# Kernel optimization log

Measured on AMD Instinct MI355X. Metric: run time of the kernel, lower is better.

The kernel has to match this reference:

```python
import jax, jax.numpy as jnp
import numpy as np

B, D, C = 4096, 1024, 11003
SCALE = 28.0
EPS_LS = 0.1
T = 4.0
L2, L3, L4 = 1.0, 1.0, 1.0
ALPHA, BETA = 0.6, 0.4
SPOS, SNEG = 10.0, 40.0
HDR_ALPHA, HDR_BETA, PLEN = 3.0, 3.0, 63


def setup_inputs() -> dict:
    key = jax.random.key(0)
    k1, k2, k3, k4, k5 = jax.random.split(key, 5)
    return {
        "visual_embed": jax.random.normal(k1, (B, D), dtype=jnp.float32),
        "textual_embed": jax.random.normal(k2, (B, D), dtype=jnp.float32),
        "labels": jax.random.randint(k3, (B,), 0, C, dtype=jnp.int64)
        if jax.config.read("jax_enable_x64") else jax.random.randint(k3, (B,), 0, C, dtype=jnp.int32),
        "W": jax.random.normal(k4, (D, C), dtype=jnp.float32) * (6.0 / (D + C)) ** 0.5,
        "W_text": jax.random.normal(k5, (D, C), dtype=jnp.float32) * (6.0 / (D + C)) ** 0.5,
    }


def _l2norm(x, axis):
    return x / jnp.linalg.norm(x, axis=axis, keepdims=True)


def _label_smooth_ce(logits, labels):
    # CrossEntropyLabelSmooth with epsilon=0.1
    lp = jax.nn.log_softmax(logits, axis=1)
    n, c = logits.shape
    picked = jnp.take_along_axis(lp, labels[:, None], axis=1)[:, 0]
    return -((1.0 - EPS_LS) * picked + (EPS_LS / c) * lp.sum(axis=1)).mean()


def _pdist(e, eps=1e-12):
    sq = (e * e).sum(axis=1)
    d2 = jnp.maximum(sq[:, None] + sq[None, :] - 2.0 * (e @ e.T), eps)
    d = jnp.sqrt(d2)
    return d * (1.0 - jnp.eye(e.shape[0], dtype=d.dtype))  # zero diagonal


def _hard_dark_rank(student, teacher):
    score_t = -HDR_ALPHA * _pdist(teacher) ** HDR_BETA
    score_s = -HDR_ALPHA * _pdist(student) ** HDR_BETA
    # top PLEN neighbors of teacher (skip self at rank 0), descending sort
    permute_idx = jnp.argsort(-score_t, axis=1)[:, 1 : PLEN + 1]  # [B, PLEN]
    ordered = jnp.take_along_axis(score_s, permute_idx, axis=1)  # [B, PLEN]
    # logsumexp over suffixes ordered[:, i:] == reversed cumulative logsumexp
    rev = jnp.flip(ordered, axis=1)
    lse_tail = jnp.flip(jax.lax.cumlogsumexp(rev, axis=1), axis=1)
    log_prob = (ordered - lse_tail).sum(axis=1)
    return (-log_prob).mean()


def _kl_div(student_logits, teacher_logits):
    s = jax.nn.softmax(student_logits / T, axis=1)
    t = jax.nn.softmax(jax.lax.stop_gradient(teacher_logits) / T, axis=1)
    log_s = jnp.log(jnp.maximum(s, 1e-12))
    log_t = jnp.log(jnp.maximum(t, 1e-12))
    return (((log_t - log_s) * t).sum(axis=1)).mean()


def reference(visual_embed, textual_embed, labels, W, W_text):
    vn = _l2norm(visual_embed, axis=1)
    tn = _l2norm(textual_embed, axis=1)
    Wn = W / jnp.linalg.norm(W, axis=0, keepdims=True)
    Wtn = W_text / jnp.linalg.norm(W_text, axis=0, keepdims=True)

    visual_logits = SCALE * (vn @ Wn)   # [B, C]
    textual_logits = SCALE * (tn @ Wn)  # [B, C]

    v_loss = _label_smooth_ce(visual_logits, labels)
    t_loss = _label_smooth_ce(textual_logits, labels)

    # distillation (LAMBDA2 feature L2 + LAMBDA3 KL on logits)
    vf = jax.lax.stop_gradient(vn)
    dist_f = ((vf - tn) ** 2).sum(axis=1).mean()
    dist_p = _kl_div(textual_logits, visual_logits)
    distillation = L2 * dist_f + L3 * dist_p

    # W_text filter CE (LAMBDA4 branch)
    t_filter = L4 * _label_smooth_ce(SCALE * (tn @ Wtn), labels)

    # HardDarkRank (Flickr30K branch): student=textual, teacher=detached visual
    loss_hdr = _hard_dark_rank(tn, jax.lax.stop_gradient(vn))

    instance = v_loss + t_loss + t_filter + distillation + 0.1 * loss_hdr

    # global_align_loss, fully vectorized. The original loops over rows AND
    # columns so every (i,j) pair is counted twice.
    sim = vn @ tn.T  # [B, B]
    mask = labels[:, None] == labels[None, :]
    loss_pos = jnp.log1p(jnp.exp(-SPOS * (sim - ALPHA)))
    loss_neg = jnp.log1p(jnp.exp(SNEG * (sim - BETA)))
    global_align = 2.0 * jnp.where(mask, loss_pos, loss_neg).sum() / sim.shape[0]

    return instance + global_align
```

## Files before the change

kernel.cpp:

```cpp
#include <hip/hip_runtime.h>
#include <math.h>

#define Bn 4096
#define Dn 1024
#define Cn 11003
#define Cpad 11008
#define NCTL 86
#define NQ 9
#define NT 32
#define NTRI 528

typedef __attribute__((ext_vector_type(8))) short bf16x8;
typedef __attribute__((ext_vector_type(4))) float f32x4;
typedef __attribute__((ext_vector_type(16))) float f32x16;

__device__ __forceinline__ unsigned short f2bf(float f) {
  union { float f; unsigned u; } v; v.f = f;
  unsigned r = (v.u + 0x7fffu + ((v.u >> 16) & 1u)) >> 16;
  return (unsigned short)r;
}
__device__ __forceinline__ float bf2f(unsigned short h) {
  union { unsigned u; float f; } v; v.u = ((unsigned)h) << 16;
  return v.f;
}

__device__ __forceinline__ void stage16(const unsigned short* g, unsigned short* l) {
  __builtin_amdgcn_global_load_lds(
      (const __attribute__((address_space(1))) void*)g,
      (__attribute__((address_space(3))) void*)l, 16, 0, 0);
}

#define SRC_BLK(tid) (((tid) & 7) ^ (((tid) >> 3) & 7))
#define FRAG(buf, R, KB) (*(const bf16x8*)((buf) + (R) * 64 + (((KB) ^ ((R) & 7)) * 8)))

__device__ __forceinline__ float blk_sum256(float v, volatile float* sb) {
#pragma unroll
  for (int o = 32; o > 0; o >>= 1) v += __shfl_down(v, o, 64);
  __syncthreads();
  if ((threadIdx.x & 63) == 0) sb[threadIdx.x >> 6] = v;
  __syncthreads();
  return sb[0] + sb[1] + sb[2] + sb[3];
}

__global__ void zero_acc_k(float* acc) {
  if (threadIdx.x < 8) acc[threadIdx.x] = 0.f;
}

__global__ __launch_bounds__(256) void rownorm_k(const float* __restrict__ xv,
                                                 const float* __restrict__ xt,
                                                 unsigned short* __restrict__ yv,
                                                 unsigned short* __restrict__ yt,
                                                 float* __restrict__ sqv,
                                                 float* __restrict__ sqt) {
  __shared__ float sb[4];
  const float* x = blockIdx.y ? xt : xv;
  unsigned short* y = blockIdx.y ? yt : yv;
  float* sq = blockIdx.y ? sqt : sqv;
  int r = blockIdx.x;
  const float* xr = x + (size_t)r * Dn;
  float s = 0.f;
  for (int k = threadIdx.x; k < Dn; k += 256) { float v = xr[k]; s += v * v; }
  s = blk_sum256(s, sb);
  float nrm = sqrtf(s);
  float s2 = 0.f;
  for (int k = threadIdx.x; k < Dn; k += 256) {
    float v = xr[k] / nrm;
    y[(size_t)r * Dn + k] = f2bf(v);
    s2 += v * v;
  }
  s2 = blk_sum256(s2, sb);
  if (threadIdx.x == 0) sq[r] = s2;
}

__global__ __launch_bounds__(256) void colnorm_k(const float* __restrict__ W,
                                                 const float* __restrict__ Wt,
                                                 float* __restrict__ rnW,
                                                 float* __restrict__ rnWt) {
  const float* X = blockIdx.y ? Wt : W;
  float* rn = blockIdx.y ? rnWt : rnW;
  int c = blockIdx.x * 256 + threadIdx.x;
  if (c >= Cn) return;
  float s = 0.f;
  for (int d = 0; d < Dn; ++d) { float v = X[(size_t)d * Cn + c]; s += v * v; }
  rn[c] = 1.f / sqrtf(s);
}

__global__ __launch_bounds__(256) void transpose_k(const float* __restrict__ W,
                                                   const float* __restrict__ Wt,
                                                   const float* __restrict__ rnW,
                                                   const float* __restrict__ rnWt,
                                                   unsigned short* __restrict__ WnT,
                                                   unsigned short* __restrict__ WtnT) {
  __shared__ float T[64][65];
  const float* X = blockIdx.z ? Wt : W;
  const float* rn = blockIdx.z ? rnWt : rnW;
  unsigned short* WT = blockIdx.z ? WtnT : WnT;
  const int c0 = blockIdx.x * 64, d0 = blockIdx.y * 64;
  const int tid = threadIdx.x;
  const int cl = tid & 63;
  for (int dl = tid >> 6; dl < 64; dl += 4) {
    float v = (c0 + cl < Cn) ? X[(size_t)(d0 + dl) * Cn + c0 + cl] : 0.f;
    T[cl][dl] = v;
  }
  __syncthreads();
  const int dd = tid & 63;
  for (int co = tid >> 6; co < 64; co += 4) {
    int c = c0 + co;
    unsigned short o = 0;
    if (c < Cn) o = f2bf(T[co][dd] * rn[c]);
    WT[(size_t)c * Dn + d0 + dd] = o;
  }
}

__global__ __launch_bounds__(256, 2) void logits_vt_k(
    const unsigned short* __restrict__ vnh, const unsigned short* __restrict__ tnh,
    const unsigned short* __restrict__ WnT, float* __restrict__ part) {
  __shared__ __align__(16) unsigned short Av[128 * 64];
  __shared__ __align__(16) unsigned short At[128 * 64];
  __shared__ __align__(16) unsigned short Bs[128 * 64];
  __shared__ float qsum[7 * 128];

  const int rt = blockIdx.x, ct = blockIdx.y;
  const int r0 = rt * 128, c0 = ct * 128;
  const int tid = threadIdx.x;
  const int lane = tid & 63;
  const int wid = tid >> 6;
  const int wr = (wid >> 1) * 64, wc = (wid & 1) * 64;
  const int l31 = lane & 31, half = lane >> 5;

  for (int t = tid; t < 7 * 128; t += 256) qsum[t] = 0.f;

  f32x16 accV[2][2], accT[2][2];
#pragma unroll
  for (int i = 0; i < 2; ++i)
#pragma unroll
    for (int j = 0; j < 2; ++j)
#pragma unroll
      for (int e = 0; e < 16; ++e) { accV[i][j][e] = 0.f; accT[i][j][e] = 0.f; }

  const int srow = tid >> 3;
  const int skc = SRC_BLK(tid) * 8;

  for (int kk = 0; kk < 16; ++kk) {
    const int k0 = kk * 64;
#pragma unroll
    for (int p = 0; p < 4; ++p) {
      stage16(vnh + (size_t)(r0 + p * 32 + srow) * Dn + k0 + skc, Av + p * 2048 + tid * 8);
      stage16(tnh + (size_t)(r0 + p * 32 + srow) * Dn + k0 + skc, At + p * 2048 + tid * 8);
      stage16(WnT + (size_t)(c0 + p * 32 + srow) * Dn + k0 + skc, Bs + p * 2048 + tid * 8);
    }
    __syncthreads();
#pragma unroll
    for (int t = 0; t < 4; ++t) {
      const int KB = t * 2 + half;
      bf16x8 av[2], at[2], bb[2];
#pragma unroll
      for (int f = 0; f < 2; ++f) {
        av[f] = FRAG(Av, wr + f * 32 + l31, KB);
        at[f] = FRAG(At, wr + f * 32 + l31, KB);
        bb[f] = FRAG(Bs, wc + f * 32 + l31, KB);
      }
#pragma unroll
      for (int i = 0; i < 2; ++i)
#pragma unroll
        for (int j = 0; j < 2; ++j) {
          accV[i][j] = __builtin_amdgcn_mfma_f32_32x32x16_bf16(av[i], bb[j], accV[i][j], 0, 0, 0);
          accT[i][j] = __builtin_amdgcn_mfma_f32_32x32x16_bf16(at[i], bb[j], accT[i][j], 0, 0, 0);
        }
    }
    __syncthreads();
  }

#pragma unroll
  for (int bi = 0; bi < 2; ++bi) {
#pragma unroll
    for (int r = 0; r < 16; ++r) {
      const int rowl = wr + bi * 32 + (r & 3) + 8 * (r >> 2) + 4 * half;
      float s0 = 0.f, s1 = 0.f, s2 = 0.f, s3 = 0.f, s6 = 0.f, s7 = 0.f, s8 = 0.f;
#pragma unroll
      for (int bj = 0; bj < 2; ++bj) {
        int col = c0 + wc + bj * 32 + l31;
        if (col < Cn) {
          float V = 28.f * accV[bi][bj][r];
          float T = 28.f * accT[bi][bj][r];
          float ev4 = __expf((V - 28.f) * 0.25f);
          float et4 = __expf((T - 28.f) * 0.25f);
          float ev2 = ev4 * ev4, et2 = et4 * et4;
          s0 += ev2 * ev2;
          s1 += V;
          s2 += et2 * et2;
          s3 += T;
          s6 += ev4;
          s7 += et4;
          s8 += ev4 * (V - T);
        }
      }
#pragma unroll
      for (int o = 1; o < 32; o <<= 1) {
        s0 += __shfl_xor(s0, o, 64); s1 += __shfl_xor(s1, o, 64);
        s2 += __shfl_xor(s2, o, 64); s3 += __shfl_xor(s3, o, 64);
        s6 += __shfl_xor(s6, o, 64); s7 += __shfl_xor(s7, o, 64);
        s8 += __shfl_xor(s8, o, 64);
      }
      if (l31 == 0) {
        atomicAdd(&qsum[0 * 128 + rowl], s0);
        atomicAdd(&qsum[1 * 128 + rowl], s1);
        atomicAdd(&qsum[2 * 128 + rowl], s2);
        atomicAdd(&qsum[3 * 128 + rowl], s3);
        atomicAdd(&qsum[4 * 128 + rowl], s6);
        atomicAdd(&qsum[5 * 128 + rowl], s7);
        atomicAdd(&qsum[6 * 128 + rowl], s8);
      }
    }
  }
  __syncthreads();
  if (tid < 128) {
    size_t base = (size_t)ct * Bn + r0 + tid;
    const size_t qs = (size_t)NCTL * Bn;
    part[0 * qs + base] = qsum[0 * 128 + tid];
    part[1 * qs + base] = qsum[1 * 128 + tid];
    part[2 * qs + base] = qsum[2 * 128 + tid];
    part[3 * qs + base] = qsum[3 * 128 + tid];
    part[6 * qs + base] = qsum[4 * 128 + tid];
    part[7 * qs + base] = qsum[5 * 128 + tid];
    part[8 * qs + base] = qsum[6 * 128 + tid];
  }
}

__global__ __launch_bounds__(256, 2) void logits_f_k(
    const unsigned short* __restrict__ tnh, const unsigned short* __restrict__ WtnT,
    float* __restrict__ part) {
  __shared__ __align__(16) unsigned short Aa[256 * 64];
  __shared__ __align__(16) unsigned short Bs[128 * 64];
  __shared__ float qsum[2 * 256];

  const int rt = blockIdx.x, ct = blockIdx.y;
  const int r0 = rt * 256, c0 = ct * 128;
  const int tid = threadIdx.x;
  const int lane = tid & 63;
  const int wid = tid >> 6;
  const int wr = (wid >> 1) * 128, wc = (wid & 1) * 64;
  const int l31 = lane & 31, half = lane >> 5;

  for (int t = tid; t < 2 * 256; t += 256) qsum[t] = 0.f;

  f32x16 acc[4][2];
#pragma unroll
  for (int i = 0; i < 4; ++i)
#pragma unroll
    for (int j = 0; j < 2; ++j)
#pragma unroll
      for (int e = 0; e < 16; ++e) acc[i][j][e] = 0.f;

  const int srow = tid >> 3;
  const int skc = SRC_BLK(tid) * 8;

  for (int kk = 0; kk < 16; ++kk) {
    const int k0 = kk * 64;
#pragma unroll
    for (int p = 0; p < 8; ++p)
      stage16(tnh + (size_t)(r0 + p * 32 + srow) * Dn + k0 + skc, Aa + p * 2048 + tid * 8);
#pragma unroll
    for (int p = 0; p < 4; ++p)
      stage16(WtnT + (size_t)(c0 + p * 32 + srow) * Dn + k0 + skc, Bs + p * 2048 + tid * 8);
    __syncthreads();
#pragma unroll
    for (int t = 0; t < 4; ++t) {
      const int KB = t * 2 + half;
      bf16x8 aa[4], bb[2];
#pragma unroll
      for (int f = 0; f < 4; ++f) aa[f] = FRAG(Aa, wr + f * 32 + l31, KB);
#pragma unroll
      for (int f = 0; f < 2; ++f) bb[f] = FRAG(Bs, wc + f * 32 + l31, KB);
#pragma unroll
      for (int i = 0; i < 4; ++i)
#pragma unroll
        for (int j = 0; j < 2; ++j)
          acc[i][j] = __builtin_amdgcn_mfma_f32_32x32x16_bf16(aa[i], bb[j], acc[i][j], 0, 0, 0);
    }
    __syncthreads();
  }

#pragma unroll
  for (int bi = 0; bi < 4; ++bi) {
#pragma unroll
    for (int r = 0; r < 16; ++r) {
      const int rowl = wr + bi * 32 + (r & 3) + 8 * (r >> 2) + 4 * half;
      float s4 = 0.f, s5 = 0.f;
#pragma unroll
      for (int bj = 0; bj < 2; ++bj) {
        int col = c0 + wc + bj * 32 + l31;
        if (col < Cn) {
          float F = 28.f * acc[bi][bj][r];
          s4 += __expf(F - 28.f);
          s5 += F;
        }
      }
#pragma unroll
      for (int o = 1; o < 32; o <<= 1) {
        s4 += __shfl_xor(s4, o, 64);
        s5 += __shfl_xor(s5, o, 64);
      }
      if (l31 == 0) {
        atomicAdd(&qsum[0 * 256 + rowl], s4);
        atomicAdd(&qsum[1 * 256 + rowl], s5);
      }
    }
  }
  __syncthreads();
  {
    size_t base = (size_t)ct * Bn + r0 + tid;
    const size_t qs = (size_t)NCTL * Bn;
    part[4 * qs + base] = qsum[0 * 256 + tid];
    part[5 * qs + base] = qsum[1 * 256 + tid];
  }
}

__global__ __launch_bounds__(256, 2) void gramv_align_k(
    const unsigned short* __restrict__ vnh, const unsigned short* __restrict__ tnh,
    const int* __restrict__ labels, float* __restrict__ G, float* __restrict__ accbuf) {
  __shared__ __align__(16) unsigned short Aa[128 * 64];
  __shared__ __align__(16) unsigned short Vb[128 * 64];
  __shared__ __align__(16) unsigned short Tb[128 * 64];
  __shared__ int li_s[128], lj_s[128];
  __shared__ float sb[4];
  const int jt = blockIdx.x, it = blockIdx.y;
  const int j0 = jt * 128, i0 = it * 128;
  const int tid = threadIdx.x;
  const int lane = tid & 63;
  const int wid = tid >> 6;
  const int wr = (wid >> 1) * 64, wc = (wid & 1) * 64;
  const int m = lane & 15, q = lane >> 4;

  if (tid < 128) li_s[tid] = labels[i0 + tid];
  else lj_s[tid - 128] = labels[j0 + tid - 128];

  const f32x4 zero4 = {0.f, 0.f, 0.f, 0.f};
  f32x4 accG[4][4], accS[4][4];
#pragma unroll
  for (int i = 0; i < 4; ++i)
#pragma unroll
    for (int j = 0; j < 4; ++j) { accG[i][j] = zero4; accS[i][j] = zero4; }

  const int srow = tid >> 3;
  const int skc = SRC_BLK(tid) * 8;

  for (int kk = 0; kk < 16; ++kk) {
    const int k0 = kk * 64;
#pragma unroll
    for (int p = 0; p < 4; ++p) {
      stage16(vnh + (size_t)(i0 + p * 32 + srow) * Dn + k0 + skc, Aa + p * 2048 + tid * 8);
      stage16(vnh + (size_t)(j0 + p * 32 + srow) * Dn + k0 + skc, Vb + p * 2048 + tid * 8);
      stage16(tnh + (size_t)(j0 + p * 32 + srow) * Dn + k0 + skc, Tb + p * 2048 + tid * 8);
    }
    __syncthreads();
#pragma unroll
    for (int ks = 0; ks < 2; ++ks) {
      const int KB = ks * 4 + q;
      bf16x8 aa[4], vb[4], tb[4];
#pragma unroll
      for (int f = 0; f < 4; ++f) {
        aa[f] = FRAG(Aa, wr + f * 16 + m, KB);
        vb[f] = FRAG(Vb, wc + f * 16 + m, KB);
        tb[f] = FRAG(Tb, wc + f * 16 + m, KB);
      }
#pragma unroll
      for (int i = 0; i < 4; ++i)
#pragma unroll
        for (int j = 0; j < 4; ++j) {
          accG[i][j] = __builtin_amdgcn_mfma_f32_16x16x32_bf16(aa[i], vb[j], accG[i][j], 0, 0, 0);
          accS[i][j] = __builtin_amdgcn_mfma_f32_16x16x32_bf16(aa[i], tb[j], accS[i][j], 0, 0, 0);
        }
    }
    __syncthreads();
  }

  float ls = 0.f;
#pragma unroll
  for (int i = 0; i < 4; ++i)
#pragma unroll
    for (int r = 0; r < 4; ++r) {
      int rowl = wr + i * 16 + q * 4 + r;
      int li = li_s[rowl];
#pragma unroll
      for (int j = 0; j < 4; ++j) {
        int coll = wc + j * 16 + m;
        G[(size_t)(i0 + rowl) * Bn + j0 + coll] = accG[i][j][r];
        int lj = lj_s[coll];
        float s = accS[i][j][r];
        float x = (li == lj) ? (-10.f * (s - 0.6f)) : (40.f * (s - 0.4f));
        ls += fmaxf(x, 0.f) + __logf(1.f + __expf(-fabsf(x)));
      }
    }
  float tot = blk_sum256(ls, sb);
  if (tid == 0) atomicAdd(&accbuf[1], tot);
}

__global__ __launch_bounds__(256, 3) void gramsym_bf16_k(const unsigned short* __restrict__ A,
                                                         unsigned short* __restrict__ G) {
  __shared__ __align__(16) unsigned short Aa[128 * 64];
  __shared__ __align__(16) unsigned short Bs[128 * 64];
  int t = blockIdx.x, it = 0, rem = NT;
  while (t >= rem) { t -= rem; ++it; --rem; }
  const int jt = it + t;
  const int i0 = it * 128, j0 = jt * 128;
  const int tid = threadIdx.x;
  const int lane = tid & 63;
  const int wid = tid >> 6;
  const int wr = (wid >> 1) * 64, wc = (wid & 1) * 64;
  const int m = lane & 15, q = lane >> 4;

  const f32x4 zero4 = {0.f, 0.f, 0.f, 0.f};
  f32x4 acc[4][4];
#pragma unroll
  for (int i = 0; i < 4; ++i)
#pragma unroll
    for (int j = 0; j < 4; ++j) acc[i][j] = zero4;

  const int srow = tid >> 3;
  const int skc = SRC_BLK(tid) * 8;

  for (int kk = 0; kk < 16; ++kk) {
    const int k0 = kk * 64;
#pragma unroll
    for (int p = 0; p < 4; ++p) {
      stage16(A + (size_t)(i0 + p * 32 + srow) * Dn + k0 + skc, Aa + p * 2048 + tid * 8);
      stage16(A + (size_t)(j0 + p * 32 + srow) * Dn + k0 + skc, Bs + p * 2048 + tid * 8);
    }
    __syncthreads();
#pragma unroll
    for (int ks = 0; ks < 2; ++ks) {
      const int KB = ks * 4 + q;
      bf16x8 aa[4], bb[4];
#pragma unroll
      for (int f = 0; f < 4; ++f) {
        aa[f] = FRAG(Aa, wr + f * 16 + m, KB);
        bb[f] = FRAG(Bs, wc + f * 16 + m, KB);
      }
#pragma unroll
      for (int i = 0; i < 4; ++i)
#pragma unroll
        for (int j = 0; j < 4; ++j)
          acc[i][j] = __builtin_amdgcn_mfma_f32_16x16x32_bf16(aa[i], bb[j], acc[i][j], 0, 0, 0);
    }
    __syncthreads();
  }
#pragma unroll
  for (int i = 0; i < 4; ++i)
#pragma unroll
    for (int j = 0; j < 4; ++j)
#pragma unroll
      for (int r = 0; r < 4; ++r) {
        int row = wr + i * 16 + q * 4 + r, col = wc + j * 16 + m;
        unsigned short h = f2bf(acc[i][j][r]);
        G[(size_t)(i0 + row) * Bn + j0 + col] = h;
        if (it != jt) G[(size_t)(j0 + col) * Bn + i0 + row] = h;
      }
}

__global__ __launch_bounds__(256) void picked_k(const unsigned short* __restrict__ vnh,
                                                const unsigned short* __restrict__ tnh,
                                                const unsigned short* __restrict__ WnT,
                                                const unsigned short* __restrict__ WtnT,
                                                const int* __restrict__ labels,
                                                float* __restrict__ pv, float* __restrict__ pt,
                                                float* __restrict__ pf, float* __restrict__ df) {
  __shared__ float sb[4];
  int r = blockIdx.x;
  int lab = labels[r];
  float spv = 0.f, spt = 0.f, spf = 0.f, sdf = 0.f;
  for (int k = threadIdx.x; k < Dn; k += 256) {
    float a = bf2f(vnh[(size_t)r * Dn + k]);
    float b = bf2f(tnh[(size_t)r * Dn + k]);
    float w = bf2f(WnT[(size_t)lab * Dn + k]);
    float wt = bf2f(WtnT[(size_t)lab * Dn + k]);
    spv += a * w;
    spt += b * w;
    spf += b * wt;
    float dd = a - b;
    sdf += dd * dd;
  }
  spv = blk_sum256(spv, sb);
  spt = blk_sum256(spt, sb);
  spf = blk_sum256(spf, sb);
  sdf = blk_sum256(sdf, sb);
  if (threadIdx.x == 0) {
    pv[r] = 28.f * spv;
    pt[r] = 28.f * spt;
    pf[r] = 28.f * spf;
    df[r] = sdf;
  }
}

__global__ __launch_bounds__(256) void finalize_k(const float* __restrict__ part,
                                                  const float* __restrict__ pv,
                                                  const float* __restrict__ pt,
                                                  const float* __restrict__ pf,
                                                  const float* __restrict__ df,
                                                  float* __restrict__ accbuf) {
  __shared__ float sb[4];
  int r = blockIdx.x * 256 + threadIdx.x;
  float s[NQ];
#pragma unroll
  for (int q = 0; q < NQ; ++q) s[q] = 0.f;
  const size_t qs = (size_t)NCTL * Bn;
  for (int ct = 0; ct < NCTL; ++ct) {
#pragma unroll
    for (int q = 0; q < NQ; ++q) s[q] += part[(size_t)q * qs + (size_t)ct * Bn + r];
  }
  float lseV = logf(s[0]) + 28.f;
  float lseT = logf(s[2]) + 28.f;
  float lseF = logf(s[4]) + 28.f;
  const float invC = 1.f / (float)Cn;
  float ceV = -(0.9f * (pv[r] - lseV) + 0.1f * invC * (s[1] - (float)Cn * lseV));
  float ceT = -(0.9f * (pt[r] - lseT) + 0.1f * invC * (s[3] - (float)Cn * lseT));
  float ceF = -(0.9f * (pf[r] - lseF) + 0.1f * invC * (s[5] - (float)Cn * lseF));
  float kl = s[8] / (4.f * s[6]) + logf(s[7]) - logf(s[6]);
  float row = ceV + ceT + ceF + kl + df[r];
  float tot = blk_sum256(row, sb);
  if (threadIdx.x == 0) atomicAdd(&accbuf[0], tot / (float)Bn);
}

__device__ __forceinline__ int kswz(int j) {
  return (j & ~63) | ((j ^ (j >> 6)) & 63);
}
__device__ __forceinline__ unsigned long long shflx_u64(unsigned long long v, int o) {
  int lo = __shfl_xor((int)(unsigned)v, o, 64);
  int hi = __shfl_xor((int)(unsigned)(v >> 32), o, 64);
  return ((unsigned long long)(unsigned)hi << 32) | (unsigned)lo;
}

__global__ __launch_bounds__(256) void hdr_k(const float* __restrict__ Gv,
                                             const unsigned short* __restrict__ Gtb,
                                             const float* __restrict__ sqv,
                                             const float* __restrict__ sqt,
                                             float* __restrict__ accbuf) {
  __shared__ float key[Bn];
  __shared__ int selIdx[64];
  __shared__ float selS[64];
  const int i = blockIdx.x, tid = threadIdx.x;
  const int lane = tid & 63, wid = tid >> 6;
  const float INF = __builtin_inff();
  float sqi = sqv[i];
  const float4* gv4 = (const float4*)(Gv + (size_t)i * Bn);
  const float4* sq4 = (const float4*)sqv;
  for (int j4 = tid; j4 < Bn / 4; j4 += 256) {
    float4 g = gv4[j4];
    float4 s = sq4[j4];
    int j = j4 * 4;
    key[kswz(j + 0)] = (j + 0 == i) ? INF : fmaxf(sqi + s.x - 2.f * g.x, 1e-12f);
    key[kswz(j + 1)] = (j + 1 == i) ? INF : fmaxf(sqi + s.y - 2.f * g.y, 1e-12f);
    key[kswz(j + 2)] = (j + 2 == i) ? INF : fmaxf(sqi + s.z - 2.f * g.z, 1e-12f);
    key[kswz(j + 3)] = (j + 3 == i) ? INF : fmaxf(sqi + s.w - 2.f * g.w, 1e-12f);
  }
  __syncthreads();

  if (wid == 0) {
    unsigned long long best = ~0ull;
    for (int k = 0; k < 64; ++k) {
      int j = k * 64 + lane;
      float v = key[kswz(j)];
      unsigned long long p = ((unsigned long long)__float_as_uint(v) << 32) | (unsigned)j;
      if (p < best) best = p;
    }
    for (int it = 0; it < 63; ++it) {
      unsigned long long w = best;
#pragma unroll
      for (int o = 32; o > 0; o >>= 1) {
        unsigned long long ow = shflx_u64(w, o);
        if (ow < w) w = ow;
      }
      int bj = (int)(unsigned)w;
      if (lane == 0) selIdx[it] = bj;
      int s = bj & 63;
      int kj = (lane << 6) | s;
      int sidx = kswz(kj);
      float kv = key[sidx];
      if (kj == bj) { kv = INF; key[sidx] = INF; }
      unsigned long long p = ((unsigned long long)__float_as_uint(kv) << 32) | (unsigned)kj;
#pragma unroll
      for (int o = 32; o > 0; o >>= 1) {
        unsigned long long op = shflx_u64(p, o);
        if (op < p) p = op;
      }
      if (lane == s) best = p;
    }
  }
  __syncthreads();

  if (tid < 63) {
    int j = selIdx[tid];
    float g = bf2f(Gtb[(size_t)i * Bn + j]);
    float d2 = fmaxf(sqt[i] + sqt[j] - 2.f * g, 1e-12f);
    selS[tid] = -3.f * sqrtf(d2) * d2;
  }
  __syncthreads();

  if (tid == 0) {
    float lse = selS[62];
    float loss = 0.f;
    for (int k = 61; k >= 0; --k) {
      float a = fmaxf(lse, selS[k]);
      lse = a + logf(__expf(lse - a) + __expf(selS[k] - a));
      loss += lse - selS[k];
    }
    atomicAdd(&accbuf[2], loss);
  }
}

__global__ void combine_k(const float* __restrict__ accbuf, float* __restrict__ out) {
  out[0] = accbuf[0] + (2.f / (float)Bn) * accbuf[1] + (0.1f / (float)Bn) * accbuf[2];
}

extern "C" void kernel_launch(void* const* d_in, const int* in_sizes, int n_in,
                              void* d_out, int out_size, void* d_ws, size_t ws_size,
                              hipStream_t stream) {
  const float* ve = (const float*)d_in[0];
  const float* te = (const float*)d_in[1];
  const int* labels = (const int*)d_in[2];
  const float* W = (const float*)d_in[3];
  const float* Wt = (const float*)d_in[4];
  float* out = (float*)d_out;

  char* base = (char*)d_ws;
  size_t off = 0;
  unsigned short* vnh = (unsigned short*)(base + off);  off += (size_t)Bn * Dn * 2;
  unsigned short* tnh = (unsigned short*)(base + off);  off += (size_t)Bn * Dn * 2;
  unsigned short* WnT = (unsigned short*)(base + off);  off += (size_t)Cpad * Dn * 2;
  unsigned short* WtnT = (unsigned short*)(base + off); off += (size_t)Cpad * Dn * 2;
  float* Gv = (float*)(base + off);          off += (size_t)Bn * Bn * 4;
  unsigned short* Gtb = (unsigned short*)(base + off); off += (size_t)Bn * Bn * 2;
  float* part = (float*)(base + off);        off += (size_t)NQ * NCTL * Bn * 4;
  float* rnW = (float*)(base + off);         off += (size_t)Cpad * 4;
  float* rnWt = (float*)(base + off);        off += (size_t)Cpad * 4;
  float* sqv = (float*)(base + off);         off += (size_t)Bn * 4;
  float* sqt = (float*)(base + off);         off += (size_t)Bn * 4;
  float* pv = (float*)(base + off);          off += (size_t)Bn * 4;
  float* pt = (float*)(base + off);          off += (size_t)Bn * 4;
  float* pf = (float*)(base + off);          off += (size_t)Bn * 4;
  float* df = (float*)(base + off);          off += (size_t)Bn * 4;
  float* acc = (float*)(base + off);         off += 64;

  zero_acc_k<<<1, 64, 0, stream>>>(acc);
  rownorm_k<<<dim3(Bn, 2), 256, 0, stream>>>(ve, te, vnh, tnh, sqv, sqt);
  colnorm_k<<<dim3((Cn + 255) / 256, 2), 256, 0, stream>>>(W, Wt, rnW, rnWt);
  transpose_k<<<dim3(Cpad / 64, Dn / 64, 2), 256, 0, stream>>>(W, Wt, rnW, rnWt, WnT, WtnT);
  logits_vt_k<<<dim3(Bn / 128, NCTL), 256, 0, stream>>>(vnh, tnh, WnT, part);
  logits_f_k<<<dim3(Bn / 256, NCTL), 256, 0, stream>>>(tnh, WtnT, part);
  gramv_align_k<<<dim3(NT, NT), 256, 0, stream>>>(vnh, tnh, labels, Gv, acc);
  gramsym_bf16_k<<<NTRI, 256, 0, stream>>>(tnh, Gtb);
  picked_k<<<Bn, 256, 0, stream>>>(vnh, tnh, WnT, WtnT, labels, pv, pt, pf, df);
  finalize_k<<<Bn / 256, 256, 0, stream>>>(part, pv, pt, pf, df, acc);
  hdr_k<<<Bn, 256, 0, stream>>>(Gv, Gtb, sqv, sqt, acc);
  combine_k<<<1, 1, 0, stream>>>(acc, out);
}
```

Before: 1.026 ms.

## Compute logit row sums via column-sum of W and switch to 16x16 MFMA

Row sums of the logits (needed for label smoothing) are now computed algebraically as the dot product of each normalized embedding with the column-sum of the bf16 normalized weight, accumulated during the transpose. This drops three per-element sum reductions and their partial buffers from the GEMM epilogues. Separately, the logits GEMMs switch from 32x32x16 to 16x16x32 MFMA tiles, which changes register layout and the epilogue shuffle width. The column-sum uses atomics and reassociates the sum, so rounding differs slightly.

```diff
diff --git a/kernel.cpp b/kernel.cpp
--- a/kernel.cpp
+++ b/kernel.cpp
@@ -6,13 +6,12 @@
 #define Cn 11003
 #define Cpad 11008
 #define NCTL 86
-#define NQ 9
+#define NQ 6
 #define NT 32
 #define NTRI 528
 
 typedef __attribute__((ext_vector_type(8))) short bf16x8;
 typedef __attribute__((ext_vector_type(4))) float f32x4;
-typedef __attribute__((ext_vector_type(16))) float f32x16;
 
 __device__ __forceinline__ unsigned short f2bf(float f) {
   union { float f; unsigned u; } v; v.f = f;
@@ -42,8 +41,10 @@
   return sb[0] + sb[1] + sb[2] + sb[3];
 }
 
-__global__ void zero_acc_k(float* acc) {
-  if (threadIdx.x < 8) acc[threadIdx.x] = 0.f;
+__global__ void zero_acc_k(float* acc, float* cw, float* cwt) {
+  int tid = threadIdx.x;
+  for (int i = tid; i < Dn; i += 256) { cw[i] = 0.f; cwt[i] = 0.f; }
+  if (tid < 8) acc[tid] = 0.f;
 }
 
 __global__ __launch_bounds__(256) void rownorm_k(const float* __restrict__ xv,
@@ -90,26 +91,36 @@
                                                    const float* __restrict__ rnW,
                                                    const float* __restrict__ rnWt,
                                                    unsigned short* __restrict__ WnT,
-                                                   unsigned short* __restrict__ WtnT) {
+                                                   unsigned short* __restrict__ WtnT,
+                                                   float* __restrict__ cw,
+                                                   float* __restrict__ cwt) {
   __shared__ float T[64][65];
+  __shared__ float cwp[64];
   const float* X = blockIdx.z ? Wt : W;
   const float* rn = blockIdx.z ? rnWt : rnW;
   unsigned short* WT = blockIdx.z ? WtnT : WnT;
+  float* cwg = blockIdx.z ? cwt : cw;
   const int c0 = blockIdx.x * 64, d0 = blockIdx.y * 64;
   const int tid = threadIdx.x;
   const int cl = tid & 63;
+  if (tid < 64) cwp[tid] = 0.f;
   for (int dl = tid >> 6; dl < 64; dl += 4) {
     float v = (c0 + cl < Cn) ? X[(size_t)(d0 + dl) * Cn + c0 + cl] : 0.f;
     T[cl][dl] = v;
   }
   __syncthreads();
   const int dd = tid & 63;
+  float ls = 0.f;
   for (int co = tid >> 6; co < 64; co += 4) {
     int c = c0 + co;
     unsigned short o = 0;
     if (c < Cn) o = f2bf(T[co][dd] * rn[c]);
     WT[(size_t)c * Dn + d0 + dd] = o;
-  }
+    ls += bf2f(o);
+  }
+  atomicAdd(&cwp[dd], ls);
+  __syncthreads();
+  if (tid < 64) atomicAdd(&cwg[d0 + tid], cwp[tid]);
 }
 
 __global__ __launch_bounds__(256, 2) void logits_vt_k(
@@ -118,7 +129,7 @@
   __shared__ __align__(16) unsigned short Av[128 * 64];
   __shared__ __align__(16) unsigned short At[128 * 64];
   __shared__ __align__(16) unsigned short Bs[128 * 64];
-  __shared__ float qsum[7 * 128];
+  __shared__ float qsum[5 * 128];
 
   const int rt = blockIdx.x, ct = blockIdx.y;
   const int r0 = rt * 128, c0 = ct * 128;
@@ -126,17 +137,16 @@
   const int lane = tid & 63;
   const int wid = tid >> 6;
   const int wr = (wid >> 1) * 64, wc = (wid & 1) * 64;
-  const int l31 = lane & 31, half = lane >> 5;
-
-  for (int t = tid; t < 7 * 128; t += 256) qsum[t] = 0.f;
-
-  f32x16 accV[2][2], accT[2][2];
-#pragma unroll
-  for (int i = 0; i < 2; ++i)
-#pragma unroll
-    for (int j = 0; j < 2; ++j)
-#pragma unroll
-      for (int e = 0; e < 16; ++e) { accV[i][j][e] = 0.f; accT[i][j][e] = 0.f; }
+  const int m = lane & 15, q = lane >> 4;
+
+  for (int t = tid; t < 5 * 128; t += 256) qsum[t] = 0.f;
+
+  const f32x4 zero4 = {0.f, 0.f, 0.f, 0.f};
+  f32x4 accV[4][4], accT[4][4];
+#pragma unroll
+  for (int i = 0; i < 4; ++i)
+#pragma unroll
+    for (int j = 0; j < 4; ++j) { accV[i][j] = zero4; accT[i][j] = zero4; }
 
   const int srow = tid >> 3;
   const int skc = SRC_BLK(tid) * 8;
@@ -151,65 +161,60 @@
     }
     __syncthreads();
 #pragma unroll
-    for (int t = 0; t < 4; ++t) {
-      const int KB = t * 2 + half;
-      bf16x8 av[2], at[2], bb[2];
-#pragma unroll
-      for (int f = 0; f < 2; ++f) {
-        av[f] = FRAG(Av, wr + f * 32 + l31, KB);
-        at[f] = FRAG(At, wr + f * 32 + l31, KB);
-        bb[f] = FRAG(Bs, wc + f * 32 + l31, KB);
-      }
-#pragma unroll
-      for (int i = 0; i < 2; ++i)
-#pragma unroll
-        for (int j = 0; j < 2; ++j) {
-          accV[i][j] = __builtin_amdgcn_mfma_f32_32x32x16_bf16(av[i], bb[j], accV[i][j], 0, 0, 0);
-          accT[i][j] = __builtin_amdgcn_mfma_f32_32x32x16_bf16(at[i], bb[j], accT[i][j], 0, 0, 0);
+    for (int ks = 0; ks < 2; ++ks) {
+      const int KB = ks * 4 + q;
+      bf16x8 av[4], at[4], bb[4];
+#pragma unroll
+      for (int f = 0; f < 4; ++f) {
+        av[f] = FRAG(Av, wr + f * 16 + m, KB);
+        at[f] = FRAG(At, wr + f * 16 + m, KB);
+        bb[f] = FRAG(Bs, wc + f * 16 + m, KB);
+      }
+#pragma unroll
+      for (int i = 0; i < 4; ++i)
+#pragma unroll
+        for (int j = 0; j < 4; ++j) {
+          accV[i][j] = __builtin_amdgcn_mfma_f32_16x16x32_bf16(av[i], bb[j], accV[i][j], 0, 0, 0);
+          accT[i][j] = __builtin_amdgcn_mfma_f32_16x16x32_bf16(at[i], bb[j], accT[i][j], 0, 0, 0);
         }
     }
     __syncthreads();
   }
 
 #pragma unroll
-  for (int bi = 0; bi < 2; ++bi) {
-#pragma unroll
-    for (int r = 0; r < 16; ++r) {
-      const int rowl = wr + bi * 32 + (r & 3) + 8 * (r >> 2) + 4 * half;
-      float s0 = 0.f, s1 = 0.f, s2 = 0.f, s3 = 0.f, s6 = 0.f, s7 = 0.f, s8 = 0.f;
-#pragma unroll
-      for (int bj = 0; bj < 2; ++bj) {
-        int col = c0 + wc + bj * 32 + l31;
+  for (int i = 0; i < 4; ++i) {
+#pragma unroll
+    for (int r = 0; r < 4; ++r) {
+      const int rowl = wr + i * 16 + q * 4 + r;
+      float s0 = 0.f, s2 = 0.f, s6 = 0.f, s7 = 0.f, s8 = 0.f;
+#pragma unroll
+      for (int j = 0; j < 4; ++j) {
+        int col = c0 + wc + j * 16 + m;
         if (col < Cn) {
-          float V = 28.f * accV[bi][bj][r];
-          float T = 28.f * accT[bi][bj][r];
+          float V = 28.f * accV[i][j][r];
+          float T = 28.f * accT[i][j][r];
           float ev4 = __expf((V - 28.f) * 0.25f);
           float et4 = __expf((T - 28.f) * 0.25f);
           float ev2 = ev4 * ev4, et2 = et4 * et4;
           s0 += ev2 * ev2;
-          s1 += V;
           s2 += et2 * et2;
-          s3 += T;
           s6 += ev4;
           s7 += et4;
           s8 += ev4 * (V - T);
         }
       }
 #pragma unroll
-      for (int o = 1; o < 32; o <<= 1) {
-        s0 += __shfl_xor(s0, o, 64); s1 += __shfl_xor(s1, o, 64);
-        s2 += __shfl_xor(s2, o, 64); s3 += __shfl_xor(s3, o, 64);
+      for (int o = 1; o < 16; o <<= 1) {
+        s0 += __shfl_xor(s0, o, 64); s2 += __shfl_xor(s2, o, 64);
         s6 += __shfl_xor(s6, o, 64); s7 += __shfl_xor(s7, o, 64);
         s8 += __shfl_xor(s8, o, 64);
       }
-      if (l31 == 0) {
+      if (m == 0) {
         atomicAdd(&qsum[0 * 128 + rowl], s0);
-        atomicAdd(&qsum[1 * 128 + rowl], s1);
-        atomicAdd(&qsum[2 * 128 + rowl], s2);
-        atomicAdd(&qsum[3 * 128 + rowl], s3);
-        atomicAdd(&qsum[4 * 128 + rowl], s6);
-        atomicAdd(&qsum[5 * 128 + rowl], s7);
-        atomicAdd(&qsum[6 * 128 + rowl], s8);
+        atomicAdd(&qsum[1 * 128 + rowl], s2);
+        atomicAdd(&qsum[2 * 128 + rowl], s6);
+        atomicAdd(&qsum[3 * 128 + rowl], s7);
+        atomicAdd(&qsum[4 * 128 + rowl], s8);
       }
     }
   }
@@ -219,11 +224,9 @@
     const size_t qs = (size_t)NCTL * Bn;
     part[0 * qs + base] = qsum[0 * 128 + tid];
     part[1 * qs + base] = qsum[1 * 128 + tid];
-    part[2 * qs + base] = qsum[2 * 128 + tid];
-    part[3 * qs + base] = qsum[3 * 128 + tid];
-    part[6 * qs + base] = qsum[4 * 128 + tid];
-    part[7 * qs + base] = qsum[5 * 128 + tid];
-    part[8 * qs + base] = qsum[6 * 128 + tid];
+    part[3 * qs + base] = qsum[2 * 128 + tid];
+    part[4 * qs + base] = qsum[3 * 128 + tid];
+    part[5 * qs + base] = qsum[4 * 128 + tid];
   }
 }
 
@@ -232,7 +235,7 @@
     float* __restrict__ part) {
   __shared__ __align__(16) unsigned short Aa[256 * 64];
   __shared__ __align__(16) unsigned short Bs[128 * 64];
-  __shared__ float qsum[2 * 256];
+  __shared__ float qsum[256];
 
   const int rt = blockIdx.x, ct = blockIdx.y;
   const int r0 = rt * 256, c0 = ct * 128;
@@ -240,17 +243,16 @@
   const int lane = tid & 63;
   const int wid = tid >> 6;
   const int wr = (wid >> 1) * 128, wc = (wid & 1) * 64;
-  const int l31 = lane & 31, half = lane >> 5;
-
-  for (int t = tid; t < 2 * 256; t += 256) qsum[t] = 0.f;
-
-  f32x16 acc[4][2];
-#pragma unroll
-  for (int i = 0; i < 4; ++i)
-#pragma unroll
-    for (int j = 0; j < 2; ++j)
-#pragma unroll
-      for (int e = 0; e < 16; ++e) acc[i][j][e] = 0.f;
+  const int m = lane & 15, q = lane >> 4;
+
+  qsum[tid] = 0.f;
+
+  const f32x4 zero4 = {0.f, 0.f, 0.f, 0.f};
+  f32x4 acc[8][4];
+#pragma unroll
+  for (int i = 0; i < 8; ++i)
+#pragma unroll
+    for (int j = 0; j < 4; ++j) acc[i][j] = zero4;
 
   const int srow = tid >> 3;
   const int skc = SRC_BLK(tid) * 8;
@@ -265,54 +267,43 @@
       stage16(WtnT + (size_t)(c0 + p * 32 + srow) * Dn + k0 + skc, Bs + p * 2048 + tid * 8);
     __syncthreads();
 #pragma unroll
-    for (int t = 0; t < 4; ++t) {
-      const int KB = t * 2 + half;
-      bf16x8 aa[4], bb[2];
-#pragma unroll
-      for (int f = 0; f < 4; ++f) aa[f] = FRAG(Aa, wr + f * 32 + l31, KB);
-#pragma unroll
-      for (int f = 0; f < 2; ++f) bb[f] = FRAG(Bs, wc + f * 32 + l31, KB);
-#pragma unroll
-      for (int i = 0; i < 4; ++i)
-#pragma unroll
-        for (int j = 0; j < 2; ++j)
-          acc[i][j] = __builtin_amdgcn_mfma_f32_32x32x16_bf16(aa[i], bb[j], acc[i][j], 0, 0, 0);
-    }
-    __syncthreads();
-  }
-
-#pragma unroll
-  for (int bi = 0; bi < 4; ++bi) {
-#pragma unroll
-    for (int r = 0; r < 16; ++r) {
-      const int rowl = wr + bi * 32 + (r & 3) + 8 * (r >> 2) + 4 * half;
-      float s4 = 0.f, s5 = 0.f;
-#pragma unroll
-      for (int bj = 0; bj < 2; ++bj) {
-        int col = c0 + wc + bj * 32 + l31;
-        if (col < Cn) {
-          float F = 28.f * acc[bi][bj][r];
-          s4 += __expf(F - 28.f);
-          s5 += F;
-        }
-      }
-#pragma unroll
-      for (int o = 1; o < 32; o <<= 1) {
-        s4 += __shfl_xor(s4, o, 64);
-        s5 += __shfl_xor(s5, o, 64);
-      }
-      if (l31 == 0) {
-        atomicAdd(&qsum[0 * 256 + rowl], s4);
-        atomicAdd(&qsum[1 * 256 + rowl], s5);
-      }
+    for (int ks = 0; ks < 2; ++ks) {
+      const int KB = ks * 4 + q;
+      bf16x8 aa[8], bb[4];
+#pragma unroll
+      for (int f = 0; f < 8; ++f) aa[f] = FRAG(Aa, wr + f * 16 + m, KB);
+#pragma unroll
+      for (int f = 0; f < 4; ++f) bb[f] = FRAG(Bs, wc + f * 16 + m, KB);
+#pragma unroll
+      for (int i = 0; i < 8; ++i)
+#pragma unroll
+        for (int j = 0; j < 4; ++j)
+          acc[i][j] = __builtin_amdgcn_mfma_f32_16x16x32_bf16(aa[i], bb[j], acc[i][j], 0, 0, 0);
+    }
+    __syncthreads();
+  }
+
+#pragma unroll
+  for (int i = 0; i < 8; ++i) {
+#pragma unroll
+    for (int r = 0; r < 4; ++r) {
+      const int rowl = wr + i * 16 + q * 4 + r;
+      float s4 = 0.f;
+#pragma unroll
+      for (int j = 0; j < 4; ++j) {
+        int col = c0 + wc + j * 16 + m;
+        if (col < Cn) s4 += __expf(28.f * acc[i][j][r] - 28.f);
+      }
+#pragma unroll
+      for (int o = 1; o < 16; o <<= 1) s4 += __shfl_xor(s4, o, 64);
+      if (m == 0) atomicAdd(&qsum[rowl], s4);
     }
   }
   __syncthreads();
   {
     size_t base = (size_t)ct * Bn + r0 + tid;
     const size_t qs = (size_t)NCTL * Bn;
-    part[4 * qs + base] = qsum[0 * 256 + tid];
-    part[5 * qs + base] = qsum[1 * 256 + tid];
+    part[2 * qs + base] = qsum[tid];
   }
 }
 
@@ -462,33 +453,47 @@
                                                 const unsigned short* __restrict__ tnh,
                                                 const unsigned short* __restrict__ WnT,
                                                 const unsigned short* __restrict__ WtnT,
+                                                const float* __restrict__ cw,
+                                                const float* __restrict__ cwt,
                                                 const int* __restrict__ labels,
                                                 float* __restrict__ pv, float* __restrict__ pt,
-                                                float* __restrict__ pf, float* __restrict__ df) {
+                                                float* __restrict__ pf, float* __restrict__ df,
+                                                float* __restrict__ sv, float* __restrict__ st,
+                                                float* __restrict__ sf) {
   __shared__ float sb[4];
   int r = blockIdx.x;
   int lab = labels[r];
-  float spv = 0.f, spt = 0.f, spf = 0.f, sdf = 0.f;
+  float spv = 0.f, spt = 0.f, spf = 0.f, sdf = 0.f, ssv = 0.f, sst = 0.f, ssf = 0.f;
   for (int k = threadIdx.x; k < Dn; k += 256) {
     float a = bf2f(vnh[(size_t)r * Dn + k]);
     float b = bf2f(tnh[(size_t)r * Dn + k]);
     float w = bf2f(WnT[(size_t)lab * Dn + k]);
     float wt = bf2f(WtnT[(size_t)lab * Dn + k]);
+    float c1 = cw[k], c2 = cwt[k];
     spv += a * w;
     spt += b * w;
     spf += b * wt;
     float dd = a - b;
     sdf += dd * dd;
+    ssv += a * c1;
+    sst += b * c1;
+    ssf += b * c2;
   }
   spv = blk_sum256(spv, sb);
   spt = blk_sum256(spt, sb);
   spf = blk_sum256(spf, sb);
   sdf = blk_sum256(sdf, sb);
+  ssv = blk_sum256(ssv, sb);
+  sst = blk_sum256(sst, sb);
+  ssf = blk_sum256(ssf, sb);
   if (threadIdx.x == 0) {
     pv[r] = 28.f * spv;
     pt[r] = 28.f * spt;
     pf[r] = 28.f * spf;
     df[r] = sdf;
+    sv[r] = 28.f * ssv;
+    st[r] = 28.f * sst;
+    sf[r] = 28.f * ssf;
   }
 }
 
@@ -497,6 +502,9 @@
                                                   const float* __restrict__ pt,
                                                   const float* __restrict__ pf,
                                                   const float* __restrict__ df,
+                                                  const float* __restrict__ sv,
+                                                  const float* __restrict__ st,
+                                                  const float* __restrict__ sf,
                                                   float* __restrict__ accbuf) {
   __shared__ float sb[4];
   int r = blockIdx.x * 256 + threadIdx.x;
@@ -509,13 +517,13 @@
     for (int q = 0; q < NQ; ++q) s[q] += part[(size_t)q * qs + (size_t)ct * Bn + r];
   }
   float lseV = logf(s[0]) + 28.f;
-  float lseT = logf(s[2]) + 28.f;
-  float lseF = logf(s[4]) + 28.f;
+  float lseT = logf(s[1]) + 28.f;
+  float lseF = logf(s[2]) + 28.f;
   const float invC = 1.f / (float)Cn;
-  float ceV = -(0.9f * (pv[r] - lseV) + 0.1f * invC * (s[1] - (float)Cn * lseV));
-  float ceT = -(0.9f * (pt[r] - lseT) + 0.1f * invC * (s[3] - (float)Cn * lseT));
-  float ceF = -(0.9f * (pf[r] - lseF) + 0.1f * invC * (s[5] - (float)Cn * lseF));
-  float kl = s[8] / (4.f * s[6]) + logf(s[7]) - logf(s[6]);
+  float ceV = -(0.9f * (pv[r] - lseV) + 0.1f * invC * (sv[r] - (float)Cn * lseV));
+  float ceT = -(0.9f * (pt[r] - lseT) + 0.1f * invC * (st[r] - (float)Cn * lseT));
+  float ceF = -(0.9f * (pf[r] - lseF) + 0.1f * invC * (sf[r] - (float)Cn * lseF));
+  float kl = s[5] / (4.f * s[3]) + logf(s[4]) - logf(s[3]);
   float row = ceV + ceT + ceF + kl + df[r];
   float tot = blk_sum256(row, sb);
   if (threadIdx.x == 0) atomicAdd(&accbuf[0], tot / (float)Bn);
@@ -633,24 +641,29 @@
   float* part = (float*)(base + off);        off += (size_t)NQ * NCTL * Bn * 4;
   float* rnW = (float*)(base + off);         off += (size_t)Cpad * 4;
   float* rnWt = (float*)(base + off);        off += (size_t)Cpad * 4;
+  float* cw = (float*)(base + off);          off += (size_t)Dn * 4;
+  float* cwt = (float*)(base + off);         off += (size_t)Dn * 4;
   float* sqv = (float*)(base + off);         off += (size_t)Bn * 4;
   float* sqt = (float*)(base + off);         off += (size_t)Bn * 4;
   float* pv = (float*)(base + off);          off += (size_t)Bn * 4;
   float* pt = (float*)(base + off);          off += (size_t)Bn * 4;
   float* pf = (float*)(base + off);          off += (size_t)Bn * 4;
   float* df = (float*)(base + off);          off += (size_t)Bn * 4;
+  float* sv = (float*)(base + off);          off += (size_t)Bn * 4;
+  float* st = (float*)(base + off);          off += (size_t)Bn * 4;
+  float* sf = (float*)(base + off);          off += (size_t)Bn * 4;
   float* acc = (float*)(base + off);         off += 64;
 
-  zero_acc_k<<<1, 64, 0, stream>>>(acc);
+  zero_acc_k<<<1, 256, 0, stream>>>(acc, cw, cwt);
   rownorm_k<<<dim3(Bn, 2), 256, 0, stream>>>(ve, te, vnh, tnh, sqv, sqt);
   colnorm_k<<<dim3((Cn + 255) / 256, 2), 256, 0, stream>>>(W, Wt, rnW, rnWt);
-  transpose_k<<<dim3(Cpad / 64, Dn / 64, 2), 256, 0, stream>>>(W, Wt, rnW, rnWt, WnT, WtnT);
+  transpose_k<<<dim3(Cpad / 64, Dn / 64, 2), 256, 0, stream>>>(W, Wt, rnW, rnWt, WnT, WtnT, cw, cwt);
   logits_vt_k<<<dim3(Bn / 128, NCTL), 256, 0, stream>>>(vnh, tnh, WnT, part);
   logits_f_k<<<dim3(Bn / 256, NCTL), 256, 0, stream>>>(tnh, WtnT, part);
   gramv_align_k<<<dim3(NT, NT), 256, 0, stream>>>(vnh, tnh, labels, Gv, acc);
   gramsym_bf16_k<<<NTRI, 256, 0, stream>>>(tnh, Gtb);
-  picked_k<<<Bn, 256, 0, stream>>>(vnh, tnh, WnT, WtnT, labels, pv, pt, pf, df);
-  finalize_k<<<Bn / 256, 256, 0, stream>>>(part, pv, pt, pf, df, acc);
+  picked_k<<<Bn, 256, 0, stream>>>(vnh, tnh, WnT, WtnT, cw, cwt, labels, pv, pt, pf, df, sv, st, sf);
+  finalize_k<<<Bn / 256, 256, 0, stream>>>(part, pv, pt, pf, df, sv, st, sf, acc);
   hdr_k<<<Bn, 256, 0, stream>>>(Gv, Gtb, sqv, sqt, acc);
   combine_k<<<1, 1, 0, stream>>>(acc, out);
 }
```

New measurement: 862.2 us. 1.19x faster.
